# Kernel tuning notes

Hardware: AMD Instinct MI355X
Metric: run time of the kernel (lower is better)

The kernel has to match this reference:

```python
import jax, jax.numpy as jnp
import numpy as np

N = 100000          # total nodes
E = 3200000         # total edges (avg degree 32)
B = 100             # num graphs
NPG = N // B        # nodes per graph (uniform -> to_dense_batch is a reshape)
D_IN, D_H, D_E, N_CLS = 128, 64, 32, 10


def setup_inputs() -> dict:
    key = jax.random.key(0)
    ks = jax.random.split(key, 12)
    x = jax.random.normal(ks[0], (N, D_IN), jnp.float32)
    # edges strictly within each graph: offset by graph block
    epg = E // B
    offs = (jnp.arange(E, dtype=jnp.int32) // epg) * NPG
    src = jax.random.randint(ks[1], (E,), 0, NPG, jnp.int32) + offs
    dst = jax.random.randint(ks[2], (E,), 0, NPG, jnp.int32) + offs
    edge_index = jnp.stack([src, dst])
    batch = jnp.repeat(jnp.arange(B, dtype=jnp.int32), NPG)

    def glorot(k, fi, fo):
        return jax.random.normal(k, (fi, fo), jnp.float32) * (1.0 / np.sqrt(fi))

    return {
        "x": x, "edge_index": edge_index, "batch": batch,
        "W_a1": glorot(ks[3], D_IN, D_H), "b_a1": jnp.zeros((D_H,), jnp.float32),
        "W_a2": glorot(ks[4], D_H, D_E),  "b_a2": jnp.zeros((D_E,), jnp.float32),
        "W_x1": glorot(ks[5], D_IN, D_H), "b_x1": jnp.zeros((D_H,), jnp.float32),
        "W_x2": glorot(ks[6], D_H, D_E),  "b_x2": jnp.zeros((D_E,), jnp.float32),
        "W_lin": glorot(ks[7], D_E * D_E, N_CLS),
        "b_lin": jnp.zeros((N_CLS,), jnp.float32),
    }


def _gcn(x, W, b, src, dst, n):
    """PyG GCNConv(improved=True): sym-norm with self-loop weight 2."""
    h = x @ W                                                   # [n, out]
    deg = jax.ops.segment_sum(jnp.ones_like(dst, h.dtype), dst, n) + 2.0
    dinv = jax.lax.rsqrt(deg)                                   # [n]
    coef = dinv[src] * dinv[dst]                                # [E]
    agg = jax.ops.segment_sum(h[src] * coef[:, None], dst, n)   # gather-scatter
    agg = agg + (2.0 * dinv * dinv)[:, None] * h                # self-loop term
    return agg + b


def _segment_softmax(v, seg, nseg):
    m = jax.ops.segment_max(v, seg, nseg)
    e = jnp.exp(v - m[seg])
    s = jax.ops.segment_sum(e, seg, nseg)
    return e / s[seg]


def reference(x, edge_index, batch, W_a1, b_a1, W_a2, b_a2,
              W_x1, b_x1, W_x2, b_x2, W_lin, b_lin):
    src, dst = edge_index[0], edge_index[1]
    n = x.shape[0]
    a1 = jax.nn.relu(_gcn(x, W_a1, b_a1, src, dst, n))
    a2 = _segment_softmax(_gcn(a1, W_a2, b_a2, src, dst, n), batch, B)
    x1 = jax.nn.relu(_gcn(x, W_x1, b_x1, src, dst, n))
    x2 = jax.nn.relu(_gcn(x1, W_x2, b_x2, src, dst, n))
    # uniform graph sizes -> to_dense_batch is a reshape (no padding needed)
    a_b = a2.reshape(B, NPG, D_E)
    x_b = x2.reshape(B, NPG, D_E)
    prods = jnp.einsum('bne,bnf->bef', a_b, x_b)   # bmm(a^T, x): [B, D_E, D_E]
    flat = prods.reshape(B, D_E * D_E)
    return jax.nn.softmax(flat @ W_lin + b_lin, axis=-1)
```

## Files before the change

kernel.cpp:

```cpp
#include <hip/hip_runtime.h>
#include <hip/hip_bf16.h>
#include <hip/hip_fp16.h>

#define N_NODES 100000
#define N_EDGES 3200000
#define NB      100
#define NPG     1000
#define EPG     32000
#define DIN     128
#define DH      64
#define DE      32
#define NCLS    10
#define CNT_BLOCKS  832
#define SORT_BLOCKS 416


typedef _Float16 h2_t __attribute__((ext_vector_type(2)));
typedef _Float16 h8_t __attribute__((ext_vector_type(8)));
typedef float    f4_t __attribute__((ext_vector_type(4)));

__device__ __forceinline__ float dot2f(unsigned a, unsigned b, float c) {
#if __has_builtin(__builtin_amdgcn_fdot2)
    return __builtin_amdgcn_fdot2(__builtin_bit_cast(h2_t, a),
                                  __builtin_bit_cast(h2_t, b), c, false);
#else
    float d;
    asm("v_dot2_f32_f16 %0, %1, %2, %3" : "=v"(d) : "v"(a), "v"(b), "v"(c));
    return d;
#endif
}

#define DOT8(rA, rB, dv)                                                        \
    acc[0] = dot2f(__builtin_amdgcn_perm(rB.x, rA.x, 0x05040100u), dv, acc[0]); \
    acc[1] = dot2f(__builtin_amdgcn_perm(rB.x, rA.x, 0x07060302u), dv, acc[1]); \
    acc[2] = dot2f(__builtin_amdgcn_perm(rB.y, rA.y, 0x05040100u), dv, acc[2]); \
    acc[3] = dot2f(__builtin_amdgcn_perm(rB.y, rA.y, 0x07060302u), dv, acc[3]); \
    acc[4] = dot2f(__builtin_amdgcn_perm(rB.z, rA.z, 0x05040100u), dv, acc[4]); \
    acc[5] = dot2f(__builtin_amdgcn_perm(rB.z, rA.z, 0x07060302u), dv, acc[5]); \
    acc[6] = dot2f(__builtin_amdgcn_perm(rB.w, rA.w, 0x05040100u), dv, acc[6]); \
    acc[7] = dot2f(__builtin_amdgcn_perm(rB.w, rA.w, 0x07060302u), dv, acc[7]);


__global__ __launch_bounds__(256) void k_cnt(const int* __restrict__ dst,
                                             int* __restrict__ cnt8) {
    __shared__ int cnt[NPG];
    int slice = blockIdx.x >> 3;
    int g = (blockIdx.x & 7) + 8 * (slice % 13);
    int sub = slice / 13;
    if (g >= NB) return;
    int t = threadIdx.x;
    for (int i = t; i < NPG; i += 256) cnt[i] = 0;
    __syncthreads();
    int ebase = g * EPG + sub * 4000, nbase = g * NPG;
    for (int i = t; i < 4000; i += 256)
        atomicAdd(&cnt[dst[ebase + i] - nbase], 1);
    __syncthreads();
    for (int i = t; i < NPG; i += 256)
        cnt8[sub * N_NODES + nbase + i] = cnt[i];
}


__global__ __launch_bounds__(1024) void k_scan(const int* __restrict__ cnt8,
                                               int* __restrict__ rowptr,
                                               float* __restrict__ dinv,
                                               unsigned short* __restrict__ dh16) {
    __shared__ int sm[1024];
    int g = (blockIdx.x & 7) + 8 * (blockIdx.x >> 3);
    if (g >= NB) return;
    int t = threadIdx.x;
    int nbase = g * NPG, ebase = g * EPG;
    int v = 0;
    if (t < NPG) {
        #pragma unroll
        for (int s8 = 0; s8 < 8; s8++) v += cnt8[s8 * N_NODES + nbase + t];
        float dv = rsqrtf((float)v + 2.0f);
        dinv[nbase + t] = dv;
        dh16[nbase + t] = __half_as_ushort(__float2half_rn(dv));
    }
    sm[t] = v;
    __syncthreads();
    for (int off = 1; off < 1024; off <<= 1) {
        int xx = (t >= off) ? sm[t - off] : 0;
        __syncthreads();
        sm[t] += xx;
        __syncthreads();
    }
    if (t < NPG)
        rowptr[nbase + t] = ebase + sm[t] - v;
    if (g == NB - 1 && t == 0) rowptr[N_NODES] = N_EDGES;
}


union SharedSG {
    struct {
        int cur[256];
        unsigned buf[10000];
    } sc;
    struct {
        __align__(16) unsigned short wt[16384];
    } ge;
};

__global__ __launch_bounds__(1024) void k_sg(const int* __restrict__ src,
                                             const int* __restrict__ dst,
                                             const float* __restrict__ x,
                                             const float* __restrict__ Wa,
                                             const float* __restrict__ Wx,
                                             const int* __restrict__ rowptr,
                                             const unsigned short* __restrict__ dh16,
                                             unsigned int* __restrict__ esrc,
                                             unsigned short* __restrict__ h16) {
    __shared__ SharedSG S;
    int t = threadIdx.x;
    if (blockIdx.x < SORT_BLOCKS) {
        int xcd = blockIdx.x & 7, slot = blockIdx.x >> 3;
        int g = xcd + 8 * (slot % 13);
        int q = slot / 13;
        if (g >= NB) return;
        int nbase = g * NPG, ebase = g * EPG;
        int n0 = q * 250;
        int base0 = rowptr[nbase + n0];
        int cap = rowptr[nbase + n0 + 250] - base0;
        if (t < 250)
            S.sc.cur[t] = rowptr[nbase + n0 + t] - base0;
        __syncthreads();
        for (int i = t; i < EPG; i += 1024) {
            int d = dst[ebase + i] - nbase - n0;
            if ((unsigned)d < 250u) {
                int s = src[ebase + i];
                int pos = atomicAdd(&S.sc.cur[d], 1);
                S.sc.buf[pos] = ((unsigned)(s - nbase) * 16) |
                                ((unsigned)dh16[s] << 16);
            }
        }
        __syncthreads();
        for (int i = t; i < cap; i += 1024)
            esrc[base0 + i] = S.sc.buf[i];
    } else {
        int b2 = blockIdx.x - SORT_BLOCKS;
        int xcd = b2 & 7, slot = b2 >> 3;
        int g = xcd + 8 * (slot >> 2);
        int chunk = slot & 3;
        if (g >= NB) return;
        int row0 = g * NPG + chunk * 250;
        {
            int cc = t & 127, kg = t >> 7;
            const float* Wp = (cc < 64) ? &Wa[cc] : &Wx[cc - 64];
            #pragma unroll
            for (int j = 0; j < 4; j++) {
                int k0 = kg * 16 + j * 4;
                union { __half h[4]; uint2 u; } pk;
                #pragma unroll
                for (int m = 0; m < 4; m++)
                    pk.h[m] = __float2half_rn(Wp[(k0 + m) * 64]);
                int byte = cc * 256 + ((2 * k0) ^ ((cc & 7) << 4));
                *(uint2*)((char*)S.ge.wt + byte) = pk.u;
            }
        }
        __syncthreads();
        int w = t >> 6, l = t & 63;
        int lr = l & 15, kq = l >> 4;
        int rowA = row0 + w * 16 + lr;
        int rA = rowA < N_NODES ? rowA : N_NODES - 1;
        const float* xr = &x[(size_t)rA * 128];
        h8_t a[4];
        #pragma unroll
        for (int kc = 0; kc < 4; kc++) {
            float4 lo = *(const float4*)&xr[kc * 32 + kq * 8];
            float4 hi = *(const float4*)&xr[kc * 32 + kq * 8 + 4];
            h8_t av;
            av[0] = (_Float16)lo.x; av[1] = (_Float16)lo.y;
            av[2] = (_Float16)lo.z; av[3] = (_Float16)lo.w;
            av[4] = (_Float16)hi.x; av[5] = (_Float16)hi.y;
            av[6] = (_Float16)hi.z; av[7] = (_Float16)hi.w;
            a[kc] = av;
        }
        f4_t acc[8] = {};
        #pragma unroll
        for (int kc = 0; kc < 4; kc++) {
            #pragma unroll
            for (int n = 0; n < 8; n++) {
                int cc = n * 16 + lr;
                int byte = cc * 256 + (((kc * 32 + kq * 8) * 2) ^ ((cc & 7) << 4));
                h8_t bf = *(h8_t*)((char*)S.ge.wt + byte);
                acc[n] = __builtin_amdgcn_mfma_f32_16x16x32_f16(a[kc], bf, acc[n], 0, 0, 0);
            }
        }
        int rowD = row0 + w * 16 + kq * 4;
        #pragma unroll
        for (int n = 0; n < 8; n++) {
            #pragma unroll
            for (int j = 0; j < 4; j++) {
                int r = rowD + j;
                if (r < N_NODES)
                    h16[(size_t)r * 128 + n * 16 + lr] =
                        __half_as_ushort(__float2half_rn(acc[n][j]));
            }
        }
    }
}


__global__ __launch_bounds__(256) void k_agg128(const unsigned short* __restrict__ h16,
                                                const int* __restrict__ rowptr,
                                                const unsigned int* __restrict__ esrc,
                                                const float* __restrict__ dinv,
                                                const float* __restrict__ ba,
                                                const float* __restrict__ bx,
                                                unsigned short* __restrict__ outB16) {
    int xcd = blockIdx.x & 7, slot = blockIdx.x >> 3;
    int gi = slot / 63, chunk = slot - gi * 63;
    int g = xcd + 8 * gi;
    if (g >= NB) return;
    int grp = threadIdx.x >> 4;
    int cl  = threadIdx.x & 15;
    int nl  = chunk * 16 + grp;
    int valid = nl < NPG;
    int nlc = valid ? nl : NPG - 1;
    int wid = g * NPG + nlc;
    const uint4* hg4 = (const uint4*)(h16 + g * NPG * 128);
    float acc[8] = {};
    union U8 { uint4 u; __half h[8]; };
    int e0 = rowptr[wid];
    int e1 = valid ? rowptr[wid + 1] : e0;
    int e = e0;
    for (; e + 8 <= e1; e += 8) {
        unsigned pv0 = esrc[e + 0], pv1 = esrc[e + 1];
        unsigned pv2 = esrc[e + 2], pv3 = esrc[e + 3];
        unsigned pv4 = esrc[e + 4], pv5 = esrc[e + 5];
        unsigned pv6 = esrc[e + 6], pv7 = esrc[e + 7];
        uint4 r0 = hg4[(pv0 & 0xffffu) + cl];
        uint4 r1 = hg4[(pv1 & 0xffffu) + cl];
        uint4 r2 = hg4[(pv2 & 0xffffu) + cl];
        uint4 r3 = hg4[(pv3 & 0xffffu) + cl];
        uint4 r4 = hg4[(pv4 & 0xffffu) + cl];
        uint4 r5 = hg4[(pv5 & 0xffffu) + cl];
        uint4 r6 = hg4[(pv6 & 0xffffu) + cl];
        uint4 r7 = hg4[(pv7 & 0xffffu) + cl];
        unsigned dA = __builtin_amdgcn_perm(pv1, pv0, 0x07060302u);
        unsigned dB = __builtin_amdgcn_perm(pv3, pv2, 0x07060302u);
        unsigned dC = __builtin_amdgcn_perm(pv5, pv4, 0x07060302u);
        unsigned dD = __builtin_amdgcn_perm(pv7, pv6, 0x07060302u);
        DOT8(r0, r1, dA);
        DOT8(r2, r3, dB);
        DOT8(r4, r5, dC);
        DOT8(r6, r7, dD);
    }
    for (; e + 2 <= e1; e += 2) {
        unsigned pv0 = esrc[e], pv1 = esrc[e + 1];
        uint4 r0 = hg4[(pv0 & 0xffffu) + cl];
        uint4 r1 = hg4[(pv1 & 0xffffu) + cl];
        unsigned dA = __builtin_amdgcn_perm(pv1, pv0, 0x07060302u);
        DOT8(r0, r1, dA);
    }
    if (e < e1) {
        unsigned pv = esrc[e];
        uint4 r = hg4[(pv & 0xffffu) + cl];
        unsigned dA = pv >> 16;
        DOT8(r, r, dA);
    }
    float di = dinv[wid];
    float sw = 2.0f * di * di;
    U8 hv; hv.u = hg4[nlc * 16 + cl];
    int cl8 = cl * 8;
    const float* bb = (cl8 < 64) ? &ba[cl8] : &bx[cl8 - 64];
    union { __half2 h[4]; uint4 q; } pk;
    #pragma unroll
    for (int k = 0; k < 4; k++) {
        float ox = fmaxf(di * acc[2 * k]     + sw * __half2float(hv.h[2 * k])     + bb[2 * k],     0.0f);
        float oy = fmaxf(di * acc[2 * k + 1] + sw * __half2float(hv.h[2 * k + 1]) + bb[2 * k + 1], 0.0f);
        pk.h[k] = __floats2half2_rn(ox, oy);
    }
    if (valid)
        *(uint4*)&outB16[(size_t)wid * 128 + cl8] = pk.q;
}


__global__ __launch_bounds__(256) void k_agg64(const unsigned short* __restrict__ g16,
                                               const int* __restrict__ rowptr,
                                               const unsigned int* __restrict__ esrc,
                                               const float* __restrict__ dinv,
                                               const float* __restrict__ ba2,
                                               const float* __restrict__ bx2,
                                               float* __restrict__ s2) {
    int xcd = blockIdx.x & 7, slot = blockIdx.x >> 3;
    int gi = slot >> 5, chunk = slot & 31;
    int g = xcd + 8 * gi;
    if (g >= NB) return;
    int grp = threadIdx.x >> 3;
    int cl  = threadIdx.x & 7;
    int nl  = chunk * 32 + grp;
    int valid = nl < NPG;
    int nlc = valid ? nl : NPG - 1;
    int wid = g * NPG + nlc;
    const uint4* gg4 = (const uint4*)(g16 + g * NPG * 64);
    float acc[8] = {};
    union U8 { uint4 u; __half h[8]; };
    int e0 = rowptr[wid];
    int e1 = valid ? rowptr[wid + 1] : e0;
    int e = e0;
    for (; e + 8 <= e1; e += 8) {
        unsigned pv0 = esrc[e + 0], pv1 = esrc[e + 1];
        unsigned pv2 = esrc[e + 2], pv3 = esrc[e + 3];
        unsigned pv4 = esrc[e + 4], pv5 = esrc[e + 5];
        unsigned pv6 = esrc[e + 6], pv7 = esrc[e + 7];
        uint4 r0 = gg4[((pv0 & 0xffffu) >> 1) + cl];
        uint4 r1 = gg4[((pv1 & 0xffffu) >> 1) + cl];
        uint4 r2 = gg4[((pv2 & 0xffffu) >> 1) + cl];
        uint4 r3 = gg4[((pv3 & 0xffffu) >> 1) + cl];
        uint4 r4 = gg4[((pv4 & 0xffffu) >> 1) + cl];
        uint4 r5 = gg4[((pv5 & 0xffffu) >> 1) + cl];
        uint4 r6 = gg4[((pv6 & 0xffffu) >> 1) + cl];
        uint4 r7 = gg4[((pv7 & 0xffffu) >> 1) + cl];
        unsigned dA = __builtin_amdgcn_perm(pv1, pv0, 0x07060302u);
        unsigned dB = __builtin_amdgcn_perm(pv3, pv2, 0x07060302u);
        unsigned dC = __builtin_amdgcn_perm(pv5, pv4, 0x07060302u);
        unsigned dD = __builtin_amdgcn_perm(pv7, pv6, 0x07060302u);
        DOT8(r0, r1, dA);
        DOT8(r2, r3, dB);
        DOT8(r4, r5, dC);
        DOT8(r6, r7, dD);
    }
    for (; e + 2 <= e1; e += 2) {
        unsigned pv0 = esrc[e], pv1 = esrc[e + 1];
        uint4 r0 = gg4[((pv0 & 0xffffu) >> 1) + cl];
        uint4 r1 = gg4[((pv1 & 0xffffu) >> 1) + cl];
        unsigned dA = __builtin_amdgcn_perm(pv1, pv0, 0x07060302u);
        DOT8(r0, r1, dA);
    }
    if (e < e1) {
        unsigned pv = esrc[e];
        uint4 r = gg4[((pv & 0xffffu) >> 1) + cl];
        unsigned dA = pv >> 16;
        DOT8(r, r, dA);
    }
    float di = dinv[wid];
    float sw = 2.0f * di * di;
    U8 hv; hv.u = gg4[nlc * 8 + cl];
    int cl8 = cl * 8;
    float o[8];
    #pragma unroll
    for (int k = 0; k < 8; k++)
        o[k] = di * acc[k] + sw * __half2float(hv.h[k]);
    if (cl8 < 32) {
        #pragma unroll
        for (int k = 0; k < 8; k++) o[k] += ba2[cl8 + k];
    } else {
        #pragma unroll
        for (int k = 0; k < 8; k++) o[k] = fmaxf(o[k] + bx2[cl8 - 32 + k], 0.0f);
    }
    if (valid) {
        *(float4*)&s2[(size_t)wid * 64 + cl8]     = make_float4(o[0], o[1], o[2], o[3]);
        *(float4*)&s2[(size_t)wid * 64 + cl8 + 4] = make_float4(o[4], o[5], o[6], o[7]);
    }
}


__global__ __launch_bounds__(256) void k_gemm2(const unsigned short* __restrict__ Bm16,
                                               const float* __restrict__ Wa2,
                                               const float* __restrict__ Wx2,
                                               unsigned short* __restrict__ g16) {
    __shared__ float xs[64][132];
    __shared__ float ws[64][68];
    int xcd = blockIdx.x & 7, slot = blockIdx.x >> 3;
    int g = xcd + 8 * (slot >> 4);
    int chunk = slot & 15;
    if (g >= NB) return;
    int row0 = g * NPG + chunk * 64;
    int t = threadIdx.x;
    for (int i = 0; i < 4; i++) {
        int idx = t + 256 * i;
        int k = idx >> 4, c4 = idx & 15, c = c4 * 4;
        float4 v;
        if (c < 32) v = *(const float4*)&Wa2[k * 32 + c];
        else        v = *(const float4*)&Wx2[k * 32 + (c - 32)];
        *(float4*)&ws[k][c] = v;
    }
    for (int i = 0; i < 4; i++) {
        int idx = t + 256 * i;
        int r = idx >> 4, c8 = idx & 15;
        int rr = row0 + r; if (rr >= N_NODES) rr = N_NODES - 1;
        union { uint4 u; __half2 h[4]; } pk;
        pk.u = *(const uint4*)&Bm16[(size_t)rr * 128 + c8 * 8];
        float2 f0 = __half22float2(pk.h[0]);
        float2 f1 = __half22float2(pk.h[1]);
        float2 f2 = __half22float2(pk.h[2]);
        float2 f3 = __half22float2(pk.h[3]);
        int cb = c8 * 8;
        *(float4*)&xs[r][cb]     = make_float4(f0.x, f0.y, f1.x, f1.y);
        *(float4*)&xs[r][cb + 4] = make_float4(f2.x, f2.y, f3.x, f3.y);
    }
    __syncthreads();
    int cg = t & 15, rg = t >> 4;
    int koff = (cg < 8) ? 0 : 64;
    float acc[4][4] = {};
    for (int k = 0; k < 64; k++) {
        float4 w = *(float4*)&ws[k][cg * 4];
        float xv[4];
        for (int i = 0; i < 4; i++) xv[i] = xs[rg * 4 + i][koff + k];
        for (int i = 0; i < 4; i++) {
            acc[i][0] += xv[i] * w.x; acc[i][1] += xv[i] * w.y;
            acc[i][2] += xv[i] * w.z; acc[i][3] += xv[i] * w.w;
        }
    }
    for (int i = 0; i < 4; i++) {
        int r = row0 + rg * 4 + i;
        if (r < N_NODES) {
            union { ushort4 u; __half2 h[2]; } pk;
            pk.h[0] = __floats2half2_rn(acc[i][0], acc[i][1]);
            pk.h[1] = __floats2half2_rn(acc[i][2], acc[i][3]);
            *(ushort4*)&g16[(size_t)r * 64 + cg * 4] = pk.u;
        }
    }
}


__global__ __launch_bounds__(512) void k_smax(const float* __restrict__ s2,
                                              float* __restrict__ gmax,
                                              float* __restrict__ sinv) {
    __shared__ float red[16][32];
    int g = (blockIdx.x & 7) + 8 * (blockIdx.x >> 3);
    if (g >= NB) return;
    int t = threadIdx.x;
    int c = t & 31, sub = t >> 5;
    size_t base = (size_t)g * NPG;
    float m = -1e30f;
    for (int n = sub; n < NPG; n += 16)
        m = fmaxf(m, s2[(base + n) * 64 + c]);
    red[sub][c] = m; __syncthreads();
    if (sub == 0) {
        for (int j = 1; j < 16; j++) m = fmaxf(m, red[j][c]);
        red[0][c] = m;
        gmax[g * 32 + c] = m;
    }
    __syncthreads();
    m = red[0][c];
    __syncthreads();
    float sum = 0.0f;
    for (int n = sub; n < NPG; n += 16)
        sum += __expf(s2[(base + n) * 64 + c] - m);
    red[sub][c] = sum; __syncthreads();
    if (sub == 0) {
        for (int j = 1; j < 16; j++) sum += red[j][c];
        sinv[g * 32 + c] = 1.0f / sum;
    }
}


__global__ __launch_bounds__(256) void k_pool(const float* __restrict__ s2,
                                              const float* __restrict__ gmax,
                                              float* __restrict__ prods) {
    __shared__ float ta[25][32];
    __shared__ float tx[25][32];
    __shared__ float gm[32];
    int xcd = blockIdx.x & 7, slot = blockIdx.x >> 3;
    int g = xcd + 8 * (slot >> 3);
    int ch = slot & 7;
    if (g >= NB) return;
    int t = threadIdx.x;
    if (t < 32) gm[t] = gmax[g * 32 + t];
    int e  = t >> 3;
    int f4 = t & 7;
    float a0 = 0.f, a1 = 0.f, a2 = 0.f, a3 = 0.f;
    int base = g * NPG + ch * 125;
    for (int n0 = 0; n0 < 125; n0 += 25) {
        __syncthreads();
        for (int i = t; i < 25 * 16; i += 256) {
            int r = i >> 4, c4 = i & 15;
            float4 v = *(const float4*)&s2[(size_t)(base + n0 + r) * 64 + c4 * 4];
            if (c4 < 8) {
                int cb = c4 * 4;
                v.x = __expf(v.x - gm[cb + 0]);
                v.y = __expf(v.y - gm[cb + 1]);
                v.z = __expf(v.z - gm[cb + 2]);
                v.w = __expf(v.w - gm[cb + 3]);
                *(float4*)&ta[r][cb] = v;
            } else {
                *(float4*)&tx[r][(c4 - 8) * 4] = v;
            }
        }
        __syncthreads();
        #pragma unroll 5
        for (int n = 0; n < 25; n++) {
            float a   = ta[n][e];
            float4 xv = *(float4*)&tx[n][f4 * 4];
            a0 += a * xv.x; a1 += a * xv.y; a2 += a * xv.z; a3 += a * xv.w;
        }
    }
    *(float4*)&prods[((size_t)(g * 8 + ch)) * 1024 + e * 32 + f4 * 4] =
        make_float4(a0, a1, a2, a3);
}


__global__ __launch_bounds__(256) void k_head(const float* __restrict__ prods,
                                              const float* __restrict__ sinv,
                                              const float* __restrict__ Wlin,
                                              const float* __restrict__ blin,
                                              float* __restrict__ out) {
    __shared__ float red[4][NCLS];
    int g = (blockIdx.x & 7) + 8 * (blockIdx.x >> 3);
    if (g >= NB) return;
    int t = threadIdx.x;
    float p[NCLS];
    for (int c = 0; c < NCLS; c++) p[c] = 0.0f;
    const float* pg = &prods[(size_t)g * 8 * 1024];
    for (int j = 0; j < 4; j++) {
        int k = t * 4 + j;
        int e = k >> 5;
        float v = 0.0f;
        #pragma unroll
        for (int q = 0; q < 8; q++) v += pg[q * 1024 + k];
        v *= sinv[g * 32 + e];
        const float* wrow = &Wlin[k * NCLS];
        for (int c = 0; c < NCLS; c++) p[c] += v * wrow[c];
    }
    for (int off = 32; off > 0; off >>= 1)
        for (int c = 0; c < NCLS; c++) p[c] += __shfl_down(p[c], off, 64);
    int wave = t >> 6, lane = t & 63;
    if (lane == 0)
        for (int c = 0; c < NCLS; c++) red[wave][c] = p[c];
    __syncthreads();
    if (t == 0) {
        float logits[NCLS]; float mx = -1e30f;
        for (int c = 0; c < NCLS; c++) {
            logits[c] = red[0][c] + red[1][c] + red[2][c] + red[3][c] + blin[c];
            mx = fmaxf(mx, logits[c]);
        }
        float s = 0.0f;
        for (int c = 0; c < NCLS; c++) { logits[c] = expf(logits[c] - mx); s += logits[c]; }
        float inv = 1.0f / s;
        for (int c = 0; c < NCLS; c++) out[g * NCLS + c] = logits[c] * inv;
    }
}


extern "C" void kernel_launch(void* const* d_in, const int* in_sizes, int n_in,
                              void* d_out, int out_size, void* d_ws, size_t ws_size,
                              hipStream_t stream) {
    const float* x    = (const float*)d_in[0];
    const int*   ei   = (const int*)d_in[1];
    const float* Wa1  = (const float*)d_in[3];
    const float* ba1  = (const float*)d_in[4];
    const float* Wa2  = (const float*)d_in[5];
    const float* ba2  = (const float*)d_in[6];
    const float* Wx1  = (const float*)d_in[7];
    const float* bx1  = (const float*)d_in[8];
    const float* Wx2  = (const float*)d_in[9];
    const float* bx2  = (const float*)d_in[10];
    const float* Wlin = (const float*)d_in[11];
    const float* blin = (const float*)d_in[12];
    float* out = (float*)d_out;

    char* w = (char*)d_ws;
    auto alloc = [&](size_t bytes) -> void* {
        void* p = (void*)w;
        w += (bytes + 255) & ~(size_t)255;
        return p;
    };
    int*            rowptr = (int*)alloc((N_NODES + 1) * sizeof(int));
    int*            cnt8   = (int*)alloc((size_t)8 * N_NODES * sizeof(int));
    float*          dinv   = (float*)alloc(N_NODES * sizeof(float));
    unsigned short* dh16   = (unsigned short*)alloc(N_NODES * sizeof(unsigned short));
    unsigned int*   esrc   = (unsigned int*)alloc((size_t)N_EDGES * sizeof(unsigned int));
    float*          gmax   = (float*)alloc(NB * DE * sizeof(float));
    float*          sinv   = (float*)alloc(NB * DE * sizeof(float));
    float*          prods  = (float*)alloc((size_t)NB * 8 * 1024 * sizeof(float));
    unsigned short* h16    = (unsigned short*)alloc((size_t)N_NODES * 128 * sizeof(unsigned short));
    unsigned short* b16    = (unsigned short*)alloc((size_t)N_NODES * 128 * sizeof(unsigned short));
    unsigned short* g16    = (unsigned short*)alloc((size_t)N_NODES * 64 * sizeof(unsigned short));
    float*          s2     = (float*)alloc((size_t)N_NODES * 64 * sizeof(float));

    const int* srcp = ei;
    const int* dstp = ei + N_EDGES;

    k_cnt<<<CNT_BLOCKS, 256, 0, stream>>>(dstp, cnt8);
    k_scan<<<8 * 13, 1024, 0, stream>>>(cnt8, rowptr, dinv, dh16);
    k_sg<<<SORT_BLOCKS + 8 * 13 * 4, 1024, 0, stream>>>(srcp, dstp, x, Wa1, Wx1,
                                                        rowptr, dh16, esrc, h16);
    k_agg128<<<8 * 13 * 63, 256, 0, stream>>>(h16, rowptr, esrc, dinv, ba1, bx1, b16);
    k_gemm2<<<8 * 13 * 16, 256, 0, stream>>>(b16, Wa2, Wx2, g16);
    k_agg64<<<8 * 13 * 32, 256, 0, stream>>>(g16, rowptr, esrc, dinv, ba2, bx2, s2);
    k_smax<<<8 * 13, 512, 0, stream>>>(s2, gmax, sinv);
    k_pool<<<8 * 13 * 8, 256, 0, stream>>>(s2, gmax, prods);
    k_head<<<8 * 13, 256, 0, stream>>>(prods, sinv, Wlin, blin, out);
}
```

Measured before the change: 303.0 us.

## Stage per-graph feature tiles in LDS for both aggregation kernels

Both gather-aggregate kernels now launch one 1024-thread block per graph half. The block first copies that half of the graph's fp16 feature rows into XOR-swizzled shared memory (128 KB for agg128, 64 KB for agg64), then gathers neighbours from LDS instead of global/L2. The aim is to replace random global gathers with LDS reads and to avoid bank conflicts through the swizzle. The trade-off is only 200 blocks on the GPU, each needing a large LDS allocation, so occupancy and load balance drop. The inner loop is also unrolled by 4 instead of 8.

```diff
diff --git a/kernel.cpp b/kernel.cpp
--- a/kernel.cpp
+++ b/kernel.cpp
@@ -39,6 +39,12 @@
     acc[5] = dot2f(__builtin_amdgcn_perm(rB.z, rA.z, 0x07060302u), dv, acc[5]); \
     acc[6] = dot2f(__builtin_amdgcn_perm(rB.w, rA.w, 0x05040100u), dv, acc[6]); \
     acc[7] = dot2f(__builtin_amdgcn_perm(rB.w, rA.w, 0x07060302u), dv, acc[7]);
+
+#define DOT4(rA, rB, dv)                                                        \
+    acc[0] = dot2f(__builtin_amdgcn_perm(rB.x, rA.x, 0x05040100u), dv, acc[0]); \
+    acc[1] = dot2f(__builtin_amdgcn_perm(rB.x, rA.x, 0x07060302u), dv, acc[1]); \
+    acc[2] = dot2f(__builtin_amdgcn_perm(rB.y, rA.y, 0x05040100u), dv, acc[2]); \
+    acc[3] = dot2f(__builtin_amdgcn_perm(rB.y, rA.y, 0x07060302u), dv, acc[3]);
 
 
 __global__ __launch_bounds__(256) void k_cnt(const int* __restrict__ dst,
@@ -201,157 +207,141 @@
 }
 
 
-__global__ __launch_bounds__(256) void k_agg128(const unsigned short* __restrict__ h16,
+__global__ __launch_bounds__(1024) void k_agg128(const unsigned short* __restrict__ h16,
+                                                 const int* __restrict__ rowptr,
+                                                 const unsigned int* __restrict__ esrc,
+                                                 const float* __restrict__ dinv,
+                                                 const float* __restrict__ ba,
+                                                 const float* __restrict__ bx,
+                                                 unsigned short* __restrict__ outB16) {
+    __shared__ uint4 hl[8192];
+    int g = blockIdx.x >> 1, hf = blockIdx.x & 1;
+    int t = threadIdx.x;
+    const uint4* hg4 = (const uint4*)(h16 + (size_t)g * NPG * 128) + hf * 8;
+    {
+        int c = t & 7, r0 = t >> 3;
+        for (int r = r0; r < NPG; r += 128)
+            hl[r * 8 + (c ^ (r & 7))] = hg4[(size_t)r * 16 + c];
+    }
+    __syncthreads();
+    int grp = t >> 3, cl = t & 7;
+    int nbase = g * NPG;
+    union U8 { uint4 u; __half h[8]; };
+    for (int n = grp; n < NPG; n += 128) {
+        int wid = nbase + n;
+        int e0 = rowptr[wid], e1 = rowptr[wid + 1];
+        float acc[8] = {};
+        int e = e0;
+        for (; e + 4 <= e1; e += 4) {
+            unsigned pv0 = esrc[e],     pv1 = esrc[e + 1];
+            unsigned pv2 = esrc[e + 2], pv3 = esrc[e + 3];
+            uint4 q0 = hl[((pv0 & 0xffffu) >> 1) + (cl ^ ((pv0 >> 4) & 7u))];
+            uint4 q1 = hl[((pv1 & 0xffffu) >> 1) + (cl ^ ((pv1 >> 4) & 7u))];
+            uint4 q2 = hl[((pv2 & 0xffffu) >> 1) + (cl ^ ((pv2 >> 4) & 7u))];
+            uint4 q3 = hl[((pv3 & 0xffffu) >> 1) + (cl ^ ((pv3 >> 4) & 7u))];
+            unsigned dA = __builtin_amdgcn_perm(pv1, pv0, 0x07060302u);
+            unsigned dB = __builtin_amdgcn_perm(pv3, pv2, 0x07060302u);
+            DOT8(q0, q1, dA);
+            DOT8(q2, q3, dB);
+        }
+        if (e + 2 <= e1) {
+            unsigned pv0 = esrc[e], pv1 = esrc[e + 1];
+            uint4 q0 = hl[((pv0 & 0xffffu) >> 1) + (cl ^ ((pv0 >> 4) & 7u))];
+            uint4 q1 = hl[((pv1 & 0xffffu) >> 1) + (cl ^ ((pv1 >> 4) & 7u))];
+            unsigned dA = __builtin_amdgcn_perm(pv1, pv0, 0x07060302u);
+            DOT8(q0, q1, dA);
+            e += 2;
+        }
+        if (e < e1) {
+            unsigned pv = esrc[e];
+            uint4 q = hl[((pv & 0xffffu) >> 1) + (cl ^ ((pv >> 4) & 7u))];
+            unsigned dA = pv >> 16;
+            DOT8(q, q, dA);
+        }
+        float di = dinv[wid];
+        float sw = 2.0f * di * di;
+        U8 hv; hv.u = hl[n * 8 + (cl ^ (n & 7))];
+        int ch = hf * 64 + cl * 8;
+        const float* bb = (ch < 64) ? &ba[ch] : &bx[ch - 64];
+        union { __half2 h2[4]; uint4 q; } pk;
+        #pragma unroll
+        for (int k = 0; k < 4; k++) {
+            float ox = fmaxf(di * acc[2 * k]     + sw * __half2float(hv.h[2 * k])     + bb[2 * k],     0.0f);
+            float oy = fmaxf(di * acc[2 * k + 1] + sw * __half2float(hv.h[2 * k + 1]) + bb[2 * k + 1], 0.0f);
+            pk.h2[k] = __floats2half2_rn(ox, oy);
+        }
+        *(uint4*)&outB16[(size_t)wid * 128 + ch] = pk.q;
+    }
+}
+
+
+__global__ __launch_bounds__(1024) void k_agg64(const unsigned short* __restrict__ g16,
                                                 const int* __restrict__ rowptr,
                                                 const unsigned int* __restrict__ esrc,
                                                 const float* __restrict__ dinv,
-                                                const float* __restrict__ ba,
-                                                const float* __restrict__ bx,
-                                                unsigned short* __restrict__ outB16) {
-    int xcd = blockIdx.x & 7, slot = blockIdx.x >> 3;
-    int gi = slot / 63, chunk = slot - gi * 63;
-    int g = xcd + 8 * gi;
-    if (g >= NB) return;
-    int grp = threadIdx.x >> 4;
-    int cl  = threadIdx.x & 15;
-    int nl  = chunk * 16 + grp;
-    int valid = nl < NPG;
-    int nlc = valid ? nl : NPG - 1;
-    int wid = g * NPG + nlc;
-    const uint4* hg4 = (const uint4*)(h16 + g * NPG * 128);
-    float acc[8] = {};
-    union U8 { uint4 u; __half h[8]; };
-    int e0 = rowptr[wid];
-    int e1 = valid ? rowptr[wid + 1] : e0;
-    int e = e0;
-    for (; e + 8 <= e1; e += 8) {
-        unsigned pv0 = esrc[e + 0], pv1 = esrc[e + 1];
-        unsigned pv2 = esrc[e + 2], pv3 = esrc[e + 3];
-        unsigned pv4 = esrc[e + 4], pv5 = esrc[e + 5];
-        unsigned pv6 = esrc[e + 6], pv7 = esrc[e + 7];
-        uint4 r0 = hg4[(pv0 & 0xffffu) + cl];
-        uint4 r1 = hg4[(pv1 & 0xffffu) + cl];
-        uint4 r2 = hg4[(pv2 & 0xffffu) + cl];
-        uint4 r3 = hg4[(pv3 & 0xffffu) + cl];
-        uint4 r4 = hg4[(pv4 & 0xffffu) + cl];
-        uint4 r5 = hg4[(pv5 & 0xffffu) + cl];
-        uint4 r6 = hg4[(pv6 & 0xffffu) + cl];
-        uint4 r7 = hg4[(pv7 & 0xffffu) + cl];
-        unsigned dA = __builtin_amdgcn_perm(pv1, pv0, 0x07060302u);
-        unsigned dB = __builtin_amdgcn_perm(pv3, pv2, 0x07060302u);
-        unsigned dC = __builtin_amdgcn_perm(pv5, pv4, 0x07060302u);
-        unsigned dD = __builtin_amdgcn_perm(pv7, pv6, 0x07060302u);
-        DOT8(r0, r1, dA);
-        DOT8(r2, r3, dB);
-        DOT8(r4, r5, dC);
-        DOT8(r6, r7, dD);
-    }
-    for (; e + 2 <= e1; e += 2) {
-        unsigned pv0 = esrc[e], pv1 = esrc[e + 1];
-        uint4 r0 = hg4[(pv0 & 0xffffu) + cl];
-        uint4 r1 = hg4[(pv1 & 0xffffu) + cl];
-        unsigned dA = __builtin_amdgcn_perm(pv1, pv0, 0x07060302u);
-        DOT8(r0, r1, dA);
-    }
-    if (e < e1) {
-        unsigned pv = esrc[e];
-        uint4 r = hg4[(pv & 0xffffu) + cl];
-        unsigned dA = pv >> 16;
-        DOT8(r, r, dA);
-    }
-    float di = dinv[wid];
-    float sw = 2.0f * di * di;
-    U8 hv; hv.u = hg4[nlc * 16 + cl];
-    int cl8 = cl * 8;
-    const float* bb = (cl8 < 64) ? &ba[cl8] : &bx[cl8 - 64];
-    union { __half2 h[4]; uint4 q; } pk;
-    #pragma unroll
-    for (int k = 0; k < 4; k++) {
-        float ox = fmaxf(di * acc[2 * k]     + sw * __half2float(hv.h[2 * k])     + bb[2 * k],     0.0f);
-        float oy = fmaxf(di * acc[2 * k + 1] + sw * __half2float(hv.h[2 * k + 1]) + bb[2 * k + 1], 0.0f);
-        pk.h[k] = __floats2half2_rn(ox, oy);
-    }
-    if (valid)
-        *(uint4*)&outB16[(size_t)wid * 128 + cl8] = pk.q;
-}
-
-
-__global__ __launch_bounds__(256) void k_agg64(const unsigned short* __restrict__ g16,
-                                               const int* __restrict__ rowptr,
-                                               const unsigned int* __restrict__ esrc,
-                                               const float* __restrict__ dinv,
-                                               const float* __restrict__ ba2,
-                                               const float* __restrict__ bx2,
-                                               float* __restrict__ s2) {
-    int xcd = blockIdx.x & 7, slot = blockIdx.x >> 3;
-    int gi = slot >> 5, chunk = slot & 31;
-    int g = xcd + 8 * gi;
-    if (g >= NB) return;
-    int grp = threadIdx.x >> 3;
-    int cl  = threadIdx.x & 7;
-    int nl  = chunk * 32 + grp;
-    int valid = nl < NPG;
-    int nlc = valid ? nl : NPG - 1;
-    int wid = g * NPG + nlc;
-    const uint4* gg4 = (const uint4*)(g16 + g * NPG * 64);
-    float acc[8] = {};
-    union U8 { uint4 u; __half h[8]; };
-    int e0 = rowptr[wid];
-    int e1 = valid ? rowptr[wid + 1] : e0;
-    int e = e0;
-    for (; e + 8 <= e1; e += 8) {
-        unsigned pv0 = esrc[e + 0], pv1 = esrc[e + 1];
-        unsigned pv2 = esrc[e + 2], pv3 = esrc[e + 3];
-        unsigned pv4 = esrc[e + 4], pv5 = esrc[e + 5];
-        unsigned pv6 = esrc[e + 6], pv7 = esrc[e + 7];
-        uint4 r0 = gg4[((pv0 & 0xffffu) >> 1) + cl];
-        uint4 r1 = gg4[((pv1 & 0xffffu) >> 1) + cl];
-        uint4 r2 = gg4[((pv2 & 0xffffu) >> 1) + cl];
-        uint4 r3 = gg4[((pv3 & 0xffffu) >> 1) + cl];
-        uint4 r4 = gg4[((pv4 & 0xffffu) >> 1) + cl];
-        uint4 r5 = gg4[((pv5 & 0xffffu) >> 1) + cl];
-        uint4 r6 = gg4[((pv6 & 0xffffu) >> 1) + cl];
-        uint4 r7 = gg4[((pv7 & 0xffffu) >> 1) + cl];
-        unsigned dA = __builtin_amdgcn_perm(pv1, pv0, 0x07060302u);
-        unsigned dB = __builtin_amdgcn_perm(pv3, pv2, 0x07060302u);
-        unsigned dC = __builtin_amdgcn_perm(pv5, pv4, 0x07060302u);
-        unsigned dD = __builtin_amdgcn_perm(pv7, pv6, 0x07060302u);
-        DOT8(r0, r1, dA);
-        DOT8(r2, r3, dB);
-        DOT8(r4, r5, dC);
-        DOT8(r6, r7, dD);
-    }
-    for (; e + 2 <= e1; e += 2) {
-        unsigned pv0 = esrc[e], pv1 = esrc[e + 1];
-        uint4 r0 = gg4[((pv0 & 0xffffu) >> 1) + cl];
-        uint4 r1 = gg4[((pv1 & 0xffffu) >> 1) + cl];
-        unsigned dA = __builtin_amdgcn_perm(pv1, pv0, 0x07060302u);
-        DOT8(r0, r1, dA);
-    }
-    if (e < e1) {
-        unsigned pv = esrc[e];
-        uint4 r = gg4[((pv & 0xffffu) >> 1) + cl];
-        unsigned dA = pv >> 16;
-        DOT8(r, r, dA);
-    }
-    float di = dinv[wid];
-    float sw = 2.0f * di * di;
-    U8 hv; hv.u = gg4[nlc * 8 + cl];
-    int cl8 = cl * 8;
-    float o[8];
-    #pragma unroll
-    for (int k = 0; k < 8; k++)
-        o[k] = di * acc[k] + sw * __half2float(hv.h[k]);
-    if (cl8 < 32) {
-        #pragma unroll
-        for (int k = 0; k < 8; k++) o[k] += ba2[cl8 + k];
-    } else {
-        #pragma unroll
-        for (int k = 0; k < 8; k++) o[k] = fmaxf(o[k] + bx2[cl8 - 32 + k], 0.0f);
-    }
-    if (valid) {
-        *(float4*)&s2[(size_t)wid * 64 + cl8]     = make_float4(o[0], o[1], o[2], o[3]);
-        *(float4*)&s2[(size_t)wid * 64 + cl8 + 4] = make_float4(o[4], o[5], o[6], o[7]);
+                                                const float* __restrict__ ba2,
+                                                const float* __restrict__ bx2,
+                                                float* __restrict__ s2) {
+    __shared__ uint2 gl[8192];
+    int g = blockIdx.x >> 1, hf = blockIdx.x & 1;
+    int t = threadIdx.x;
+    const uint2* gg2 = (const uint2*)(g16 + (size_t)g * NPG * 64) + hf * 8;
+    {
+        int c = t & 7, r0 = t >> 3;
+        for (int r = r0; r < NPG; r += 128)
+            gl[r * 8 + (c ^ (r & 7))] = gg2[(size_t)r * 16 + c];
+    }
+    __syncthreads();
+    int grp = t >> 3, cl = t & 7;
+    int nbase = g * NPG;
+    union U4 { uint2 u; __half h[4]; };
+    for (int n = grp; n < NPG; n += 128) {
+        int wid = nbase + n;
+        int e0 = rowptr[wid], e1 = rowptr[wid + 1];
+        float acc[4] = {};
+        int e = e0;
+        for (; e + 4 <= e1; e += 4) {
+            unsigned pv0 = esrc[e],     pv1 = esrc[e + 1];
+            unsigned pv2 = esrc[e + 2], pv3 = esrc[e + 3];
+            uint2 q0 = gl[((pv0 & 0xffffu) >> 1) + (cl ^ ((pv0 >> 4) & 7u))];
+            uint2 q1 = gl[((pv1 & 0xffffu) >> 1) + (cl ^ ((pv1 >> 4) & 7u))];
+            uint2 q2 = gl[((pv2 & 0xffffu) >> 1) + (cl ^ ((pv2 >> 4) & 7u))];
+            uint2 q3 = gl[((pv3 & 0xffffu) >> 1) + (cl ^ ((pv3 >> 4) & 7u))];
+            unsigned dA = __builtin_amdgcn_perm(pv1, pv0, 0x07060302u);
+            unsigned dB = __builtin_amdgcn_perm(pv3, pv2, 0x07060302u);
+            DOT4(q0, q1, dA);
+            DOT4(q2, q3, dB);
+        }
+        if (e + 2 <= e1) {
+            unsigned pv0 = esrc[e], pv1 = esrc[e + 1];
+            uint2 q0 = gl[((pv0 & 0xffffu) >> 1) + (cl ^ ((pv0 >> 4) & 7u))];
+            uint2 q1 = gl[((pv1 & 0xffffu) >> 1) + (cl ^ ((pv1 >> 4) & 7u))];
+            unsigned dA = __builtin_amdgcn_perm(pv1, pv0, 0x07060302u);
+            DOT4(q0, q1, dA);
+            e += 2;
+        }
+        if (e < e1) {
+            unsigned pv = esrc[e];
+            uint2 q = gl[((pv & 0xffffu) >> 1) + (cl ^ ((pv >> 4) & 7u))];
+            unsigned dA = pv >> 16;
+            DOT4(q, q, dA);
+        }
+        float di = dinv[wid];
+        float sw = 2.0f * di * di;
+        U4 hv; hv.u = gl[n * 8 + (cl ^ (n & 7))];
+        int ch = hf * 32 + cl * 4;
+        float o[4];
+        #pragma unroll
+        for (int k = 0; k < 4; k++)
+            o[k] = di * acc[k] + sw * __half2float(hv.h[k]);
+        if (hf == 0) {
+            #pragma unroll
+            for (int k = 0; k < 4; k++) o[k] += ba2[ch + k];
+        } else {
+            #pragma unroll
+            for (int k = 0; k < 4; k++) o[k] = fmaxf(o[k] + bx2[ch - 32 + k], 0.0f);
+        }
+        *(float4*)&s2[(size_t)wid * 64 + ch] = make_float4(o[0], o[1], o[2], o[3]);
     }
 }
 
@@ -577,9 +567,9 @@
     k_scan<<<8 * 13, 1024, 0, stream>>>(cnt8, rowptr, dinv, dh16);
     k_sg<<<SORT_BLOCKS + 8 * 13 * 4, 1024, 0, stream>>>(srcp, dstp, x, Wa1, Wx1,
                                                         rowptr, dh16, esrc, h16);
-    k_agg128<<<8 * 13 * 63, 256, 0, stream>>>(h16, rowptr, esrc, dinv, ba1, bx1, b16);
+    k_agg128<<<2 * NB, 1024, 0, stream>>>(h16, rowptr, esrc, dinv, ba1, bx1, b16);
     k_gemm2<<<8 * 13 * 16, 256, 0, stream>>>(b16, Wa2, Wx2, g16);
-    k_agg64<<<8 * 13 * 32, 256, 0, stream>>>(g16, rowptr, esrc, dinv, ba2, bx2, s2);
+    k_agg64<<<2 * NB, 1024, 0, stream>>>(g16, rowptr, esrc, dinv, ba2, bx2, s2);
     k_smax<<<8 * 13, 512, 0, stream>>>(s2, gmax, sinv);
     k_pool<<<8 * 13 * 8, 256, 0, stream>>>(s2, gmax, prods);
     k_head<<<8 * 13, 256, 0, stream>>>(prods, sinv, Wlin, blin, out);
```

Result: slower. 330.7 us (+9.1%).
